# Optimization experiments

Measured on AMD Instinct MI355X. Metric: run time of the kernel, lower is better.

The kernel has to match this reference:

```python
import jax, jax.numpy as jnp
import numpy as np
from jax import lax

B, T, D, H, L = 128, 512, 256, 256, 2


def setup_inputs() -> dict:
    key = jax.random.key(0)
    ks = jax.random.split(key, 8)
    s = 1.0 / np.sqrt(H)
    return {
        "input1": jax.random.normal(ks[0], (B, T, D), jnp.float32),
        "input2": jax.random.normal(ks[1], (B, T, D), jnp.float32),
        "W_ih": jax.random.normal(ks[2], (L, 4 * H, D), jnp.float32) * s,
        "W_hh": jax.random.normal(ks[3], (L, 4 * H, H), jnp.float32) * s,
        "b_ih": jax.random.normal(ks[4], (L, 4 * H), jnp.float32) * s,
        "b_hh": jax.random.normal(ks[5], (L, 4 * H), jnp.float32) * s,
        "fc_w": jax.random.normal(ks[6], (5, H), jnp.float32) * s,
        "fc_b": jax.random.normal(ks[7], (5,), jnp.float32) * s,
    }


def _lstm_layer(x, Wih, Whh, bih, bhh):
    # x: [B, T, in]; returns (outputs [B, T, H], final h [B, H])
    b = x.shape[0]
    # precompute input projection for all timesteps (one big GEMM)
    xg = jnp.einsum('bti,gi->btg', x, Wih) + bih + bhh  # [B, T, 4H]
    h0 = jnp.zeros((b, H), x.dtype)
    c0 = jnp.zeros((b, H), x.dtype)

    def step(carry, xg_t):
        h, c = carry
        gates = xg_t + h @ Whh.T  # [B, 4H]
        i, f, g, o = jnp.split(gates, 4, axis=-1)
        i = jax.nn.sigmoid(i)
        f = jax.nn.sigmoid(f)
        g = jnp.tanh(g)
        o = jax.nn.sigmoid(o)
        c = f * c + i * g
        h = o * jnp.tanh(c)
        return (h, c), h

    (h_last, _), hs = lax.scan(step, (h0, c0), jnp.swapaxes(xg, 0, 1))
    return jnp.swapaxes(hs, 0, 1), h_last


def _forward_once(x, W_ih, W_hh, b_ih, b_hh, fc_w, fc_b):
    h_finals = []
    out = x
    for l in range(L):
        out, h_last = _lstm_layer(out, W_ih[l], W_hh[l], b_ih[l], b_hh[l])
        h_finals.append(h_last)
    hn = jnp.stack(h_finals, axis=0).reshape(-1, H)  # [L*B, H] (torch hn.view)
    return jax.nn.relu(hn) @ fc_w.T + fc_b  # [L*B, 5]


def reference(input1, input2, W_ih, W_hh, b_ih, b_hh, fc_w, fc_b):
    out1 = _forward_once(input1, W_ih, W_hh, b_ih, b_hh, fc_w, fc_b)
    out2 = _forward_once(input2, W_ih, W_hh, b_ih, b_hh, fc_w, fc_b)
    return (out1, out2)
```

## Files before the change

kernel.cpp:

```cpp
#include <hip/hip_runtime.h>
#include <hip/hip_fp16.h>

typedef unsigned int  u32;
typedef unsigned short u16;

typedef _Float16 h2v __attribute__((ext_vector_type(2)));
typedef _Float16 h4v __attribute__((ext_vector_type(4)));
typedef float    f4v __attribute__((ext_vector_type(4)));

static __device__ __forceinline__ u16 f2h_bits(float x){
    _Float16 h = (_Float16)x;
    return __builtin_bit_cast(u16, h);
}
static __device__ __forceinline__ u32 pack2(float a, float b){
    return (u32)f2h_bits(a) | ((u32)f2h_bits(b) << 16);
}
static __device__ __forceinline__ float fdot2(u32 w, u32 h, float acc){
#if __has_builtin(__builtin_amdgcn_fdot2)
    return __builtin_amdgcn_fdot2(__builtin_bit_cast(h2v, w),
                                  __builtin_bit_cast(h2v, h), acc, false);
#else
    h2v wv = __builtin_bit_cast(h2v, w), hv = __builtin_bit_cast(h2v, h);
    return acc + (float)wv[0]*(float)hv[0] + (float)wv[1]*(float)hv[1];
#endif
}
static __device__ __forceinline__ float sigm(float x){
    return 1.f / (1.f + __expf(-x));
}
static __device__ __forceinline__ float tanh_fast(float x){
    return 1.f - 2.f / (__expf(2.f*x) + 1.f);
}


__global__ void cvt_weights(const float* __restrict__ Wih,
                            const float* __restrict__ Whh,
                            const float* __restrict__ bih,
                            const float* __restrict__ bhh,
                            u32* __restrict__ wih16u,
                            u32* __restrict__ whhT,
                            float* __restrict__ bias){
    u32 e = blockIdx.x * blockDim.x + threadIdx.x;
    {
        float2 v = ((const float2*)Wih)[e];
        wih16u[e] = pack2(v.x, v.y);
    }
    {
        u32 l = e >> 17, rem = e & 131071u;
        u32 p = rem >> 10, r = rem & 1023u;
        float2 v = ((const float2*)Whh)[(size_t)(l*1024u + r)*128u + p];
        whhT[e] = pack2(v.x, v.y);
    }
    if (e < 2048u) bias[e] = bih[e] + bhh[e];
}

template<int A_FP32>
__global__ __launch_bounds__(256) void proj_gemm(
        const float* __restrict__ in1, const float* __restrict__ in2,
        const u16*  __restrict__ A16,
        const u16*  __restrict__ Bw,
        u16*        __restrict__ Cout,
        int t0, int lgTc){
    __shared__ u16 Blds[128][260];
    const int tid = threadIdx.x;
    const int n0 = blockIdx.x * 128;
    const int m0 = blockIdx.y * 128;

    {
        const u32* src = (const u32*)Bw;
        #pragma unroll
        for (int i = 0; i < 64; i++){
            int idx = i*256 + tid;
            int r  = idx >> 7;
            int cu = idx & 127;
            u32 v = src[(size_t)(n0 + r)*128 + cu];
            *(u32*)&Blds[r][cu*2] = v;
        }
    }
    __syncthreads();

    const int l   = tid & 63;
    const int wid = tid >> 6;
    const int wm = (wid >> 1) * 64;
    const int wn = (wid & 1) * 64;
    const int lr = l & 15;
    const int lk = l >> 4;

    f4v acc[4][4] = {};

    const float* a32[4];
    const u16*   a16[4];
    #pragma unroll
    for (int f = 0; f < 4; f++){
        int m = m0 + wm + f*16 + lr;
        if (A_FP32){
            int beta = m >> lgTc;
            int tc   = m & ((1 << lgTc) - 1);
            const float* base = (beta < 128) ? in1 : in2;
            a32[f] = base + ((size_t)(beta & 127)*512 + (size_t)(t0 + tc))*256;
        } else {
            a16[f] = A16 + (size_t)m*256;
        }
    }

    for (int k0 = 0; k0 < 256; k0 += 16){
        uint2 a_[4], b_[4];
        #pragma unroll
        for (int f = 0; f < 4; f++){
            if (A_FP32){
                float4 v = *(const float4*)(a32[f] + k0 + lk*4);
                a_[f] = make_uint2(pack2(v.x, v.y), pack2(v.z, v.w));
            } else {
                a_[f] = *(const uint2*)(a16[f] + k0 + lk*4);
            }
        }
        #pragma unroll
        for (int f = 0; f < 4; f++)
            b_[f] = *(const uint2*)&Blds[wn + f*16 + lr][k0 + lk*4];
        #pragma unroll
        for (int fm = 0; fm < 4; fm++)
            #pragma unroll
            for (int fn = 0; fn < 4; fn++)
                acc[fm][fn] = __builtin_amdgcn_mfma_f32_16x16x16f16(
                    __builtin_bit_cast(h4v, a_[fm]),
                    __builtin_bit_cast(h4v, b_[fn]),
                    acc[fm][fn], 0, 0, 0);
    }

    #pragma unroll
    for (int fm = 0; fm < 4; fm++){
        #pragma unroll
        for (int i = 0; i < 4; i++){
            int m = m0 + wm + fm*16 + lk*4 + i;
            size_t rowoff = (size_t)m*1024 + n0 + wn;
            #pragma unroll
            for (int fn = 0; fn < 4; fn++)
                Cout[rowoff + fn*16 + lr] = f2h_bits(acc[fm][fn][i]);
        }
    }
}

#define NREG 92
#define NLDSP 36

__global__ __launch_bounds__(1024, 4) void lstm_rec(
        const u16* __restrict__ xg,
        const u32* __restrict__ whhT,
        const float* __restrict__ bias,
        u16* __restrict__ hseq,
        u16* __restrict__ h_state,
        float* __restrict__ c_state,
        int Tc, int write_seq, int first){
    __shared__ u32 wlds[1024][NLDSP];
    __shared__ alignas(16) u16 hbuf[256];
    __shared__ float gbuf[1024];

    const int L    = threadIdx.x;
    const int beta = blockIdx.x;

    u32 w[NREG];
    #pragma unroll
    for (int p = 0; p < NREG; p++)
        w[p] = whhT[(size_t)p*1024 + L];
    #pragma unroll
    for (int i = 0; i < NLDSP; i++)
        wlds[L][i] = whhT[(size_t)(NREG + i)*1024 + L];

    const float bs = bias[L];
    float c = 0.f;
    if (L < 256){
        hbuf[L] = first ? (u16)0 : h_state[(size_t)beta*256 + L];
        if (!first) c = c_state[(size_t)beta*256 + L];
    }
    __syncthreads();

    const u16* xr = xg + (size_t)beta * Tc * 1024 + L;
    u16 xcur = xr[0];

    for (int tc = 0; tc < Tc; tc++){
        u16 xnext = (tc + 1 < Tc) ? xr[(size_t)(tc+1)*1024] : (u16)0;

        float accA = bs + (float)__builtin_bit_cast(_Float16, xcur);
        float accB = 0.f;

        const uint4* hv = (const uint4*)hbuf;
        const uint4* wl = (const uint4*)&wlds[L][0];
        #pragma unroll
        for (int q = 0; q < 23; q++){
            uint4 hh = hv[q];
            accA = fdot2(w[4*q+0], hh.x, accA);
            accB = fdot2(w[4*q+1], hh.y, accB);
            accA = fdot2(w[4*q+2], hh.z, accA);
            accB = fdot2(w[4*q+3], hh.w, accB);
        }
        #pragma unroll
        for (int j = 0; j < 9; j++){
            uint4 hh = hv[23 + j];
            uint4 ww = wl[j];
            accA = fdot2(ww.x, hh.x, accA);
            accB = fdot2(ww.y, hh.y, accB);
            accA = fdot2(ww.z, hh.z, accA);
            accB = fdot2(ww.w, hh.w, accB);
        }
        gbuf[L] = accA + accB;
        xcur = xnext;
        __syncthreads();

        if (L < 256){
            float gi = gbuf[L],       gf = gbuf[256+L];
            float gg = gbuf[512+L],   go = gbuf[768+L];
            float iv = sigm(gi), fv = sigm(gf), gv = tanh_fast(gg), ov = sigm(go);
            c = fv*c + iv*gv;
            float h = ov * tanh_fast(c);
            u16 hb = f2h_bits(h);
            hbuf[L] = hb;
            if (write_seq) hseq[((size_t)beta*Tc + tc)*256 + L] = hb;
        }
        __syncthreads();
    }

    if (L < 256){
        h_state[(size_t)beta*256 + L] = hbuf[L];
        c_state[(size_t)beta*256 + L] = c;
    }
}

__global__ void fc_out(const u16* __restrict__ hlast,
                       const float* __restrict__ fcw,
                       const float* __restrict__ fcb,
                       float* __restrict__ out){
    int r = blockIdx.x;
    int lane = threadIdx.x;
    int inp = r >> 8, rem = r & 255, l = rem >> 7, b = rem & 127;
    int beta = inp*128 + b;
    const u16* h = hlast + ((size_t)l*256 + beta)*256;

    int j0 = lane * 4;
    uint2 hb = *(const uint2*)(h + j0);
    h2v p0 = __builtin_bit_cast(h2v, hb.x), p1 = __builtin_bit_cast(h2v, hb.y);
    float hv0 = fmaxf((float)p0[0], 0.f);
    float hv1 = fmaxf((float)p0[1], 0.f);
    float hv2 = fmaxf((float)p1[0], 0.f);
    float hv3 = fmaxf((float)p1[1], 0.f);

    float acc[5];
    #pragma unroll
    for (int k = 0; k < 5; k++){
        float4 w = *(const float4*)(fcw + k*256 + j0);
        acc[k] = hv0*w.x + hv1*w.y + hv2*w.z + hv3*w.w;
    }
    #pragma unroll
    for (int k = 0; k < 5; k++)
        #pragma unroll
        for (int off = 32; off > 0; off >>= 1)
            acc[k] += __shfl_xor(acc[k], off);
    if (lane == 0){
        #pragma unroll
        for (int k = 0; k < 5; k++)
            out[(size_t)r*5 + k] = acc[k] + fcb[k];
    }
}

extern "C" void kernel_launch(void* const* d_in, const int* in_sizes, int n_in,
                              void* d_out, int out_size, void* d_ws, size_t ws_size,
                              hipStream_t stream) {
    const float* in1 = (const float*)d_in[0];
    const float* in2 = (const float*)d_in[1];
    const float* Wih = (const float*)d_in[2];
    const float* Whh = (const float*)d_in[3];
    const float* bih = (const float*)d_in[4];
    const float* bhh = (const float*)d_in[5];
    const float* fcw = (const float*)d_in[6];
    const float* fcb = (const float*)d_in[7];
    float* out = (float*)d_out;

    char* ws = (char*)d_ws;
    u16*   wih16   = (u16*)  (ws + 0x000000);
    u32*   whhT    = (u32*)  (ws + 0x100000);
    float* bias    = (float*)(ws + 0x200000);
    u16*   h_state = (u16*)  (ws + 0x202000);
    float* c_state = (float*)(ws + 0x242000);
    const size_t chunk_off = 0x300000;

    int Tc = 8;
    for (int cand = 512; cand >= 8; cand >>= 1){
        if (chunk_off + (size_t)cand * 655360ull <= ws_size){ Tc = cand; break; }
    }
    int lgTc = 31 - __builtin_clz((u32)Tc);
    u16* xgc = (u16*)(ws + chunk_off);
    u16* hsc = (u16*)(ws + chunk_off + (size_t)Tc * 524288ull);

    cvt_weights<<<1024, 256, 0, stream>>>(Wih, Whh, bih, bhh,
                                          (u32*)wih16, whhT, bias);

    const int nch = 512 / Tc;
    dim3 pg(8, 2*Tc);
    for (int k = 0; k < nch; k++){
        int t0 = k * Tc;
        proj_gemm<1><<<pg, 256, 0, stream>>>(in1, in2, (const u16*)nullptr,
                                             wih16, xgc, t0, lgTc);
        lstm_rec<<<256, 1024, 0, stream>>>((const u16*)xgc, whhT, bias,
                                           hsc, h_state, c_state,
                                           Tc, 1, k == 0);
        proj_gemm<0><<<pg, 256, 0, stream>>>((const float*)nullptr, (const float*)nullptr,
                                             (const u16*)hsc,
                                             wih16 + 262144, xgc, 0, lgTc);
        lstm_rec<<<256, 1024, 0, stream>>>((const u16*)xgc, whhT + 131072, bias + 1024,
                                           (u16*)nullptr, h_state + 65536, c_state + 65536,
                                           Tc, 0, k == 0);
    }
    fc_out<<<512, 64, 0, stream>>>(h_state, fcw, fcb, out);
}
```

Measured before the change: 2.782 ms.

## Interleave gate rows so LSTM cell update uses lane shuffles and one barrier

Permutes the recurrent weight rows, bias and the projected-input columns so that the four gates of each hidden unit sit on four adjacent lanes. Each thread applies its own activation, then lane shuffles gather i/f/g/o, which removes the gate buffer in shared memory and its extra barrier. Double-buffering the hidden state leaves one __syncthreads per timestep. In exchange every thread now runs the activation code, and three of every four lanes compute a discarded tanh.

```diff
diff --git a/kernel.cpp b/kernel.cpp
--- a/kernel.cpp
+++ b/kernel.cpp
@@ -23,12 +23,6 @@
     h2v wv = __builtin_bit_cast(h2v, w), hv = __builtin_bit_cast(h2v, h);
     return acc + (float)wv[0]*(float)hv[0] + (float)wv[1]*(float)hv[1];
 #endif
-}
-static __device__ __forceinline__ float sigm(float x){
-    return 1.f / (1.f + __expf(-x));
-}
-static __device__ __forceinline__ float tanh_fast(float x){
-    return 1.f - 2.f / (__expf(2.f*x) + 1.f);
 }
 
 
@@ -46,11 +40,16 @@
     }
     {
         u32 l = e >> 17, rem = e & 131071u;
-        u32 p = rem >> 10, r = rem & 1023u;
-        float2 v = ((const float2*)Whh)[(size_t)(l*1024u + r)*128u + p];
+        u32 p = rem >> 10, Ls = rem & 1023u;
+        u32 src = ((Ls & 3u) << 8) | (Ls >> 2);
+        float2 v = ((const float2*)Whh)[(size_t)(l*1024u + src)*128u + p];
         whhT[e] = pack2(v.x, v.y);
     }
-    if (e < 2048u) bias[e] = bih[e] + bhh[e];
+    if (e < 2048u){
+        u32 l = e >> 10, Ls = e & 1023u;
+        u32 src = l*1024u + (((Ls & 3u) << 8) | (Ls >> 2));
+        bias[e] = bih[src] + bhh[src];
+    }
 }
 
 template<int A_FP32>
@@ -131,10 +130,13 @@
         #pragma unroll
         for (int i = 0; i < 4; i++){
             int m = m0 + wm + fm*16 + lk*4 + i;
-            size_t rowoff = (size_t)m*1024 + n0 + wn;
+            size_t rowoff = (size_t)m*1024;
             #pragma unroll
-            for (int fn = 0; fn < 4; fn++)
-                Cout[rowoff + fn*16 + lr] = f2h_bits(acc[fm][fn][i]);
+            for (int fn = 0; fn < 4; fn++){
+                int n = n0 + wn + fn*16 + lr;
+                int np = ((n & 255) << 2) | (n >> 8);
+                Cout[rowoff + np] = f2h_bits(acc[fm][fn][i]);
+            }
         }
     }
 }
@@ -151,10 +153,11 @@
         float* __restrict__ c_state,
         int Tc, int write_seq, int first){
     __shared__ u32 wlds[1024][NLDSP];
-    __shared__ alignas(16) u16 hbuf[256];
-    __shared__ float gbuf[1024];
+    __shared__ alignas(16) u16 hbuf[2][256];
 
     const int L    = threadIdx.x;
+    const int q    = L & 3;
+    const int j    = L >> 2;
     const int beta = blockIdx.x;
 
     u32 w[NREG];
@@ -167,9 +170,9 @@
 
     const float bs = bias[L];
     float c = 0.f;
-    if (L < 256){
-        hbuf[L] = first ? (u16)0 : h_state[(size_t)beta*256 + L];
-        if (!first) c = c_state[(size_t)beta*256 + L];
+    if (q == 0){
+        hbuf[0][j] = first ? (u16)0 : h_state[(size_t)beta*256 + j];
+        if (!first) c = c_state[(size_t)beta*256 + j];
     }
     __syncthreads();
 
@@ -182,45 +185,53 @@
         float accA = bs + (float)__builtin_bit_cast(_Float16, xcur);
         float accB = 0.f;
 
-        const uint4* hv = (const uint4*)hbuf;
+        const uint4* hv = (const uint4*)hbuf[tc & 1];
         const uint4* wl = (const uint4*)&wlds[L][0];
         #pragma unroll
-        for (int q = 0; q < 23; q++){
-            uint4 hh = hv[q];
-            accA = fdot2(w[4*q+0], hh.x, accA);
-            accB = fdot2(w[4*q+1], hh.y, accB);
-            accA = fdot2(w[4*q+2], hh.z, accA);
-            accB = fdot2(w[4*q+3], hh.w, accB);
-        }
-        #pragma unroll
-        for (int j = 0; j < 9; j++){
-            uint4 hh = hv[23 + j];
-            uint4 ww = wl[j];
+        for (int p = 0; p < 23; p++){
+            uint4 hh = hv[p];
+            accA = fdot2(w[4*p+0], hh.x, accA);
+            accB = fdot2(w[4*p+1], hh.y, accB);
+            accA = fdot2(w[4*p+2], hh.z, accA);
+            accB = fdot2(w[4*p+3], hh.w, accB);
+        }
+        #pragma unroll
+        for (int p = 0; p < 9; p++){
+            uint4 hh = hv[23 + p];
+            uint4 ww = wl[p];
             accA = fdot2(ww.x, hh.x, accA);
             accB = fdot2(ww.y, hh.y, accB);
             accA = fdot2(ww.z, hh.z, accA);
             accB = fdot2(ww.w, hh.w, accB);
         }
-        gbuf[L] = accA + accB;
+        float acc = accA + accB;
+
+        float targ = (q == 2) ? 2.f*acc : -acc;
+        float e1 = __expf(targ);
+        float rr = 1.f / (1.f + e1);
+        float a  = (q == 2) ? 1.f - 2.f*rr : rr;
+
+        float p1 = __shfl_xor(a, 1);
+        float p2 = __shfl_xor(a, 2);
+        float p3 = __shfl_xor(p1, 2);
+
+        c = (q == 0) ? (p1*c + a*p2) : 0.f;
+        float e2 = __expf(2.f*c);
+        float th = 1.f - 2.f/(e2 + 1.f);
+        float h  = p3 * th;
+        u16 hb = f2h_bits(h);
+
+        if (q == 0){
+            hbuf[(tc & 1) ^ 1][j] = hb;
+            if (write_seq) hseq[((size_t)beta*Tc + tc)*256 + j] = hb;
+        }
         xcur = xnext;
         __syncthreads();
-
-        if (L < 256){
-            float gi = gbuf[L],       gf = gbuf[256+L];
-            float gg = gbuf[512+L],   go = gbuf[768+L];
-            float iv = sigm(gi), fv = sigm(gf), gv = tanh_fast(gg), ov = sigm(go);
-            c = fv*c + iv*gv;
-            float h = ov * tanh_fast(c);
-            u16 hb = f2h_bits(h);
-            hbuf[L] = hb;
-            if (write_seq) hseq[((size_t)beta*Tc + tc)*256 + L] = hb;
-        }
-        __syncthreads();
-    }
-
-    if (L < 256){
-        h_state[(size_t)beta*256 + L] = hbuf[L];
-        c_state[(size_t)beta*256 + L] = c;
+    }
+
+    if (q == 0){
+        h_state[(size_t)beta*256 + j] = hbuf[Tc & 1][j];
+        c_state[(size_t)beta*256 + j] = c;
     }
 }
 
```

Result: slower. 3.062 ms (+10.1%).
